# Optimization experiments

Hardware: AMD Instinct MI355X
Metric: run time of the kernel (lower is better)

The kernel has to match this reference:

```python
import jax, jax.numpy as jnp
import numpy as np


def setup_inputs() -> dict:
    key = jax.random.key(0)
    k1, k2, k3, k4 = jax.random.split(key, 4)
    B, S, E = 8, 4096, 1024
    H, D = 256, 4  # num_heads, n_wires_per_head; H*D == E
    scale = 1.0 / np.sqrt(E)
    return {
        "x": jax.random.normal(k1, (B, S, E), dtype=jnp.float32),
        "W_proj": jax.random.normal(k2, (E, E), dtype=jnp.float32) * scale,
        "W_combine": jax.random.normal(k3, (E, E), dtype=jnp.float32) * scale,
        "phi": jax.random.normal(k4, (H, D), dtype=jnp.float32),
    }


def reference(x, W_proj, W_combine, phi):
    # Linear projection (no bias): torch Linear computes x @ W.T
    proj = jnp.einsum("bse,fe->bsf", x, W_proj)  # [B,S,E]
    B, S, E = proj.shape
    H, D = phi.shape
    # Quantum head per token: RX-encode each feature, trainable RX, PauliZ measure.
    # RX(a)RX(b) = RX(a+b); <0|RX(t)^dag Z RX(t)|0> = cos(t)  =>  cos(x + phi)
    qout = jnp.cos(proj.reshape(B, S, H, D) + phi)  # broadcast phi[h,d]
    qout = qout.reshape(B, S, E)
    return jnp.einsum("bse,fe->bsf", qout, W_combine)
```

## Files before the change

### kernel.cpp

```cpp
#include <hip/hip_runtime.h>
#include <cstdint>
#include <cstddef>


typedef __attribute__((ext_vector_type(8))) short short8;
typedef __attribute__((ext_vector_type(4))) float f32x4;

__device__ __forceinline__ unsigned short f2bf(float f) {
  unsigned u = __float_as_uint(f);
  u += 0x7FFFu + ((u >> 16) & 1u);
  return (unsigned short)(u >> 16);
}

__device__ __forceinline__ void async_load16(const void* g, const void* l) {
  __builtin_amdgcn_global_load_lds(
      (const __attribute__((address_space(1))) void*)g,
      (__attribute__((address_space(3))) void*)l,
      16, 0, 0);
}

__global__ __launch_bounds__(256) void cast_all(
    const float* __restrict__ x, const float* __restrict__ Wp,
    const float* __restrict__ Wc, unsigned short* __restrict__ xb,
    unsigned short* __restrict__ wpb, unsigned short* __restrict__ wcb) {
  long i = ((long)blockIdx.x * 256 + threadIdx.x) * 4;
  const float* s;
  unsigned short* d;
  long j;
  if (i < 33554432)      { s = x;  d = xb;  j = i; }
  else if (i < 34603008) { s = Wp; d = wpb; j = i - 33554432; }
  else                   { s = Wc; d = wcb; j = i - 34603008; }
  const float4 v = *(const float4*)(s + j);
  ushort4 o;
  o.x = f2bf(v.x); o.y = f2bf(v.y); o.z = f2bf(v.z); o.w = f2bf(v.w);
  *(ushort4*)(d + j) = o;
}

constexpr int BM = 256, BN = 256, BK = 64;
constexpr int Kdim = 1024, Ndim = 1024;
constexpr int KT = Kdim / BK;

template <int EPI>
__global__ __launch_bounds__(512, 2) void gemm256(
    const unsigned short* __restrict__ A,
    const unsigned short* __restrict__ B,
    const float* __restrict__ phi,
    void* __restrict__ Cout) {
  __shared__ unsigned short As[2][2][256][32];
  __shared__ unsigned short Bs[2][2][256][32];

  const int tid    = threadIdx.x;
  const int lane   = tid & 63;
  const int wv     = tid >> 6;
  const int wr     = wv >> 2;
  const int wc     = wv & 3;
  const int lane15 = lane & 15;
  const int quad   = lane >> 4;
  const int swz8   = (quad ^ ((lane15 >> 1) & 3)) * 8;

  const int wg   = ((blockIdx.x & 7) << 6) | (blockIdx.x >> 3);
  const long row0 = (long)(wg >> 2) * BM;
  const int  col0 = (wg & 3) * BN;

  const int rsub  = lane >> 2;
  const int csrc8 = ((lane & 3) ^ ((lane >> 3) & 3)) * 8;
  const int rA    = wv * 32 + rsub;

#define STAGE(KTIDX, NB)                                                      \
  {                                                                           \
    const unsigned short* ga0 = A + (row0 + rA) * Kdim + (KTIDX) * BK + csrc8;\
    const unsigned short* ga1 = ga0 + (long)16 * Kdim;                        \
    const unsigned short* gb0 =                                               \
        B + (long)(col0 + rA) * Kdim + (KTIDX) * BK + csrc8;                  \
    const unsigned short* gb1 = gb0 + (long)16 * Kdim;                        \
    _Pragma("unroll")                                                         \
    for (int kh = 0; kh < 2; ++kh) {                                          \
      async_load16(ga0 + kh * 32, &As[NB][kh][wv * 32][0]);                   \
      async_load16(ga1 + kh * 32, &As[NB][kh][wv * 32 + 16][0]);              \
      async_load16(gb0 + kh * 32, &Bs[NB][kh][wv * 32][0]);                   \
      async_load16(gb1 + kh * 32, &Bs[NB][kh][wv * 32 + 16][0]);              \
    }                                                                         \
  }

  f32x4 acc[8][4];
#pragma unroll
  for (int i = 0; i < 8; ++i)
#pragma unroll
    for (int n = 0; n < 4; ++n) {
      f32x4 z = {0.f, 0.f, 0.f, 0.f};
      acc[i][n] = z;
    }

  STAGE(0, 0);
  asm volatile("s_waitcnt vmcnt(4)" ::: "memory");
  __builtin_amdgcn_s_barrier();

#pragma unroll 2
  for (int kt = 0; kt < KT; ++kt) {
    const int cur = kt & 1;
    short8 af[4], bfr[4];

#pragma unroll
    for (int i = 0; i < 4; ++i)
      af[i] = *(const short8*)(&As[cur][0][wr * 128 + i * 16 + lane15][swz8]);
#pragma unroll
    for (int i = 0; i < 4; ++i)
      bfr[i] = *(const short8*)(&Bs[cur][0][wc * 64 + i * 16 + lane15][swz8]);
    if (kt + 1 < KT) STAGE(kt + 1, cur ^ 1);
    __builtin_amdgcn_s_barrier();
    asm volatile("s_waitcnt lgkmcnt(0)" ::: "memory");
    __builtin_amdgcn_sched_barrier(0);
    __builtin_amdgcn_s_setprio(1);
#pragma unroll
    for (int i = 0; i < 4; ++i)
#pragma unroll
      for (int n = 0; n < 4; ++n)
        acc[i][n] = __builtin_amdgcn_mfma_f32_16x16x32_bf16(
            af[i], bfr[n], acc[i][n], 0, 0, 0);
    __builtin_amdgcn_s_setprio(0);
    __builtin_amdgcn_sched_barrier(0);
    __builtin_amdgcn_s_barrier();

#pragma unroll
    for (int i = 0; i < 4; ++i)
      af[i] =
          *(const short8*)(&As[cur][0][wr * 128 + (4 + i) * 16 + lane15][swz8]);
    __builtin_amdgcn_s_barrier();
    asm volatile("s_waitcnt lgkmcnt(0)" ::: "memory");
    __builtin_amdgcn_sched_barrier(0);
    __builtin_amdgcn_s_setprio(1);
#pragma unroll
    for (int i = 0; i < 4; ++i)
#pragma unroll
      for (int n = 0; n < 4; ++n)
        acc[4 + i][n] = __builtin_amdgcn_mfma_f32_16x16x32_bf16(
            af[i], bfr[n], acc[4 + i][n], 0, 0, 0);
    __builtin_amdgcn_s_setprio(0);
    __builtin_amdgcn_sched_barrier(0);
    if (kt == KT - 1) {
      asm volatile("s_waitcnt vmcnt(0)" ::: "memory");
    } else {
      asm volatile("s_waitcnt vmcnt(8)" ::: "memory");
    }
    __builtin_amdgcn_s_barrier();

#pragma unroll
    for (int i = 0; i < 4; ++i)
      af[i] = *(const short8*)(&As[cur][1][wr * 128 + i * 16 + lane15][swz8]);
#pragma unroll
    for (int i = 0; i < 4; ++i)
      bfr[i] = *(const short8*)(&Bs[cur][1][wc * 64 + i * 16 + lane15][swz8]);
    __builtin_amdgcn_s_barrier();
    asm volatile("s_waitcnt lgkmcnt(0)" ::: "memory");
    __builtin_amdgcn_sched_barrier(0);
    __builtin_amdgcn_s_setprio(1);
#pragma unroll
    for (int i = 0; i < 4; ++i)
#pragma unroll
      for (int n = 0; n < 4; ++n)
        acc[i][n] = __builtin_amdgcn_mfma_f32_16x16x32_bf16(
            af[i], bfr[n], acc[i][n], 0, 0, 0);
    __builtin_amdgcn_s_setprio(0);
    __builtin_amdgcn_sched_barrier(0);
    __builtin_amdgcn_s_barrier();

#pragma unroll
    for (int i = 0; i < 4; ++i)
      af[i] =
          *(const short8*)(&As[cur][1][wr * 128 + (4 + i) * 16 + lane15][swz8]);
    __builtin_amdgcn_s_barrier();
    asm volatile("s_waitcnt lgkmcnt(0)" ::: "memory");
    __builtin_amdgcn_sched_barrier(0);
    __builtin_amdgcn_s_setprio(1);
#pragma unroll
    for (int i = 0; i < 4; ++i)
#pragma unroll
      for (int n = 0; n < 4; ++n)
        acc[4 + i][n] = __builtin_amdgcn_mfma_f32_16x16x32_bf16(
            af[i], bfr[n], acc[4 + i][n], 0, 0, 0);
    __builtin_amdgcn_s_setprio(0);
    __builtin_amdgcn_sched_barrier(0);
    if (kt < KT - 1) {
      asm volatile("s_waitcnt vmcnt(4)" ::: "memory");
    }
    __builtin_amdgcn_s_barrier();
  }
#undef STAGE

  if (EPI == 1) {
    unsigned short* Q = (unsigned short*)Cout;
    float ph[4];
#pragma unroll
    for (int n = 0; n < 4; ++n)
      ph[n] = phi[col0 + wc * 64 + n * 16 + lane15];
#pragma unroll
    for (int mi = 0; mi < 8; ++mi) {
      const long rbase = row0 + wr * 128 + mi * 16 + quad * 4;
#pragma unroll
      for (int n = 0; n < 4; ++n) {
        const int c = col0 + wc * 64 + n * 16 + lane15;
#pragma unroll
        for (int r = 0; r < 4; ++r) {
          float v = __cosf(acc[mi][n][r] + ph[n]);
          Q[(rbase + r) * Ndim + c] = f2bf(v);
        }
      }
    }
  } else {
    float* C = (float*)Cout;
#pragma unroll
    for (int mi = 0; mi < 8; ++mi) {
      const long rbase = row0 + wr * 128 + mi * 16 + quad * 4;
#pragma unroll
      for (int n = 0; n < 4; ++n) {
        const int c = col0 + wc * 64 + n * 16 + lane15;
#pragma unroll
        for (int r = 0; r < 4; ++r)
          C[(rbase + r) * Ndim + c] = acc[mi][n][r];
      }
    }
  }
}

extern "C" void kernel_launch(void* const* d_in, const int* in_sizes, int n_in,
                              void* d_out, int out_size, void* d_ws, size_t ws_size,
                              hipStream_t stream) {
  const float* x   = (const float*)d_in[0];
  const float* Wp  = (const float*)d_in[1];
  const float* Wc  = (const float*)d_in[2];
  const float* phi = (const float*)d_in[3];
  float* out = (float*)d_out;

  char* ws = (char*)d_ws;
  unsigned short* Abf  = (unsigned short*)(ws);
  unsigned short* Qbf  = (unsigned short*)(ws + (size_t)67108864);
  unsigned short* Wpbf = (unsigned short*)(ws + (size_t)134217728);
  unsigned short* Wcbf = (unsigned short*)(ws + (size_t)136314880);

  cast_all<<<34816, 256, 0, stream>>>(x, Wp, Wc, Abf, Wpbf, Wcbf);
  gemm256<1><<<512, 512, 0, stream>>>(Abf, Wpbf, phi, (void*)Qbf);
  gemm256<0><<<512, 512, 0, stream>>>(Qbf, Wcbf, nullptr, (void*)out);

  (void)in_sizes; (void)n_in; (void)out_size; (void)ws_size;
}
```

Baseline: 396.6 us.

## Interleave K-half global loads across MFMA phases and grid-stride the cast kernel

The GEMM prefetch is split into per-half A and B loads that are issued across the four MFMA phases of each iteration. The first half of tile kt+2 is loaded into the buffer that was just consumed, so loads run deeper and are spread more evenly against compute, with vmcnt waits retuned to match. The cast kernel becomes a grid-stride loop over 4096 blocks that converts 8 floats per thread per iteration. The finer-grained wait counts carry correctness risk if any count is wrong.

```diff
diff --git a/kernel.cpp b/kernel.cpp
--- a/kernel.cpp
+++ b/kernel.cpp
@@ -23,17 +23,24 @@
     const float* __restrict__ x, const float* __restrict__ Wp,
     const float* __restrict__ Wc, unsigned short* __restrict__ xb,
     unsigned short* __restrict__ wpb, unsigned short* __restrict__ wcb) {
-  long i = ((long)blockIdx.x * 256 + threadIdx.x) * 4;
-  const float* s;
-  unsigned short* d;
-  long j;
-  if (i < 33554432)      { s = x;  d = xb;  j = i; }
-  else if (i < 34603008) { s = Wp; d = wpb; j = i - 33554432; }
-  else                   { s = Wc; d = wcb; j = i - 34603008; }
-  const float4 v = *(const float4*)(s + j);
-  ushort4 o;
-  o.x = f2bf(v.x); o.y = f2bf(v.y); o.z = f2bf(v.z); o.w = f2bf(v.w);
-  *(ushort4*)(d + j) = o;
+  const long nvec = 35651584 / 8;
+  for (long v = (long)blockIdx.x * 256 + threadIdx.x; v < nvec;
+       v += (long)gridDim.x * 256) {
+    const long i = v * 8;
+    const float* s;
+    unsigned short* d;
+    long j;
+    if (i < 33554432)      { s = x;  d = xb;  j = i; }
+    else if (i < 34603008) { s = Wp; d = wpb; j = i - 33554432; }
+    else                   { s = Wc; d = wcb; j = i - 34603008; }
+    const float4 a = *(const float4*)(s + j);
+    const float4 b = *(const float4*)(s + j + 4);
+    ushort4 o0, o1;
+    o0.x = f2bf(a.x); o0.y = f2bf(a.y); o0.z = f2bf(a.z); o0.w = f2bf(a.w);
+    o1.x = f2bf(b.x); o1.y = f2bf(b.y); o1.z = f2bf(b.z); o1.w = f2bf(b.w);
+    *(ushort4*)(d + j) = o0;
+    *(ushort4*)(d + j + 4) = o1;
+  }
 }
 
 constexpr int BM = 256, BN = 256, BK = 64;
@@ -62,24 +69,22 @@
   const long row0 = (long)(wg >> 2) * BM;
   const int  col0 = (wg & 3) * BN;
 
-  const int rsub  = lane >> 2;
   const int csrc8 = ((lane & 3) ^ ((lane >> 3) & 3)) * 8;
-  const int rA    = wv * 32 + rsub;
-
-#define STAGE(KTIDX, NB)                                                      \
-  {                                                                           \
-    const unsigned short* ga0 = A + (row0 + rA) * Kdim + (KTIDX) * BK + csrc8;\
-    const unsigned short* ga1 = ga0 + (long)16 * Kdim;                        \
-    const unsigned short* gb0 =                                               \
-        B + (long)(col0 + rA) * Kdim + (KTIDX) * BK + csrc8;                  \
-    const unsigned short* gb1 = gb0 + (long)16 * Kdim;                        \
-    _Pragma("unroll")                                                         \
-    for (int kh = 0; kh < 2; ++kh) {                                          \
-      async_load16(ga0 + kh * 32, &As[NB][kh][wv * 32][0]);                   \
-      async_load16(ga1 + kh * 32, &As[NB][kh][wv * 32 + 16][0]);              \
-      async_load16(gb0 + kh * 32, &Bs[NB][kh][wv * 32][0]);                   \
-      async_load16(gb1 + kh * 32, &Bs[NB][kh][wv * 32 + 16][0]);              \
-    }                                                                         \
+  const int rA    = wv * 32 + (lane >> 2);
+
+#define SA(KT2, NB, KH)                                                        \
+  {                                                                            \
+    const unsigned short* g_ =                                                 \
+        A + (row0 + rA) * Kdim + (KT2) * BK + (KH) * 32 + csrc8;               \
+    async_load16(g_, &As[NB][KH][wv * 32][0]);                                 \
+    async_load16(g_ + 16 * Kdim, &As[NB][KH][wv * 32 + 16][0]);                \
+  }
+#define SB(KT2, NB, KH)                                                        \
+  {                                                                            \
+    const unsigned short* g_ =                                                 \
+        B + (long)(col0 + rA) * Kdim + (KT2) * BK + (KH) * 32 + csrc8;         \
+    async_load16(g_, &Bs[NB][KH][wv * 32][0]);                                 \
+    async_load16(g_ + 16 * Kdim, &Bs[NB][KH][wv * 32 + 16][0]);                \
   }
 
   f32x4 acc[8][4];
@@ -91,13 +96,18 @@
       acc[i][n] = z;
     }
 
-  STAGE(0, 0);
-  asm volatile("s_waitcnt vmcnt(4)" ::: "memory");
+  SA(0, 0, 0); SB(0, 0, 0);
+  SA(0, 0, 1);
+  SB(0, 0, 1);
+  SA(1, 1, 0);
+  SB(1, 1, 0);
+  asm volatile("s_waitcnt vmcnt(8)" ::: "memory");
   __builtin_amdgcn_s_barrier();
 
 #pragma unroll 2
   for (int kt = 0; kt < KT; ++kt) {
     const int cur = kt & 1;
+    const int nxt = cur ^ 1;
     short8 af[4], bfr[4];
 
 #pragma unroll
@@ -106,7 +116,7 @@
 #pragma unroll
     for (int i = 0; i < 4; ++i)
       bfr[i] = *(const short8*)(&Bs[cur][0][wc * 64 + i * 16 + lane15][swz8]);
-    if (kt + 1 < KT) STAGE(kt + 1, cur ^ 1);
+    if (kt + 1 < KT) SA(kt + 1, nxt, 1)
     __builtin_amdgcn_s_barrier();
     asm volatile("s_waitcnt lgkmcnt(0)" ::: "memory");
     __builtin_amdgcn_sched_barrier(0);
@@ -125,6 +135,7 @@
     for (int i = 0; i < 4; ++i)
       af[i] =
           *(const short8*)(&As[cur][0][wr * 128 + (4 + i) * 16 + lane15][swz8]);
+    if (kt + 1 < KT) SB(kt + 1, nxt, 1)
     __builtin_amdgcn_s_barrier();
     asm volatile("s_waitcnt lgkmcnt(0)" ::: "memory");
     __builtin_amdgcn_sched_barrier(0);
@@ -137,10 +148,10 @@
             af[i], bfr[n], acc[4 + i][n], 0, 0, 0);
     __builtin_amdgcn_s_setprio(0);
     __builtin_amdgcn_sched_barrier(0);
-    if (kt == KT - 1) {
+    if (kt < KT - 1) {
+      asm volatile("s_waitcnt vmcnt(8)" ::: "memory");
+    } else {
       asm volatile("s_waitcnt vmcnt(0)" ::: "memory");
-    } else {
-      asm volatile("s_waitcnt vmcnt(8)" ::: "memory");
     }
     __builtin_amdgcn_s_barrier();
 
@@ -150,6 +161,7 @@
 #pragma unroll
     for (int i = 0; i < 4; ++i)
       bfr[i] = *(const short8*)(&Bs[cur][1][wc * 64 + i * 16 + lane15][swz8]);
+    if (kt + 2 < KT) SA(kt + 2, cur, 0)
     __builtin_amdgcn_s_barrier();
     asm volatile("s_waitcnt lgkmcnt(0)" ::: "memory");
     __builtin_amdgcn_sched_barrier(0);
@@ -168,6 +180,7 @@
     for (int i = 0; i < 4; ++i)
       af[i] =
           *(const short8*)(&As[cur][1][wr * 128 + (4 + i) * 16 + lane15][swz8]);
+    if (kt + 2 < KT) SB(kt + 2, cur, 0)
     __builtin_amdgcn_s_barrier();
     asm volatile("s_waitcnt lgkmcnt(0)" ::: "memory");
     __builtin_amdgcn_sched_barrier(0);
@@ -180,12 +193,15 @@
             af[i], bfr[n], acc[4 + i][n], 0, 0, 0);
     __builtin_amdgcn_s_setprio(0);
     __builtin_amdgcn_sched_barrier(0);
-    if (kt < KT - 1) {
+    if (kt < KT - 2) {
+      asm volatile("s_waitcnt vmcnt(8)" ::: "memory");
+    } else if (kt == KT - 2) {
       asm volatile("s_waitcnt vmcnt(4)" ::: "memory");
     }
     __builtin_amdgcn_s_barrier();
   }
-#undef STAGE
+#undef SA
+#undef SB
 
   if (EPI == 1) {
     unsigned short* Q = (unsigned short*)Cout;
@@ -237,7 +253,7 @@
   unsigned short* Wpbf = (unsigned short*)(ws + (size_t)134217728);
   unsigned short* Wcbf = (unsigned short*)(ws + (size_t)136314880);
 
-  cast_all<<<34816, 256, 0, stream>>>(x, Wp, Wc, Abf, Wpbf, Wcbf);
+  cast_all<<<4096, 256, 0, stream>>>(x, Wp, Wc, Abf, Wpbf, Wcbf);
   gemm256<1><<<512, 512, 0, stream>>>(Abf, Wpbf, phi, (void*)Qbf);
   gemm256<0><<<512, 512, 0, stream>>>(Qbf, Wcbf, nullptr, (void*)out);
 
```

Result: faster. 383.8 us (-3.2%).
